# Optimization experiments

Hardware: AMD Instinct MI355X
Metric: run time of the kernel (lower is better)

The kernel has to match this reference:

```python
import jax, jax.numpy as jnp
import numpy as np

EPS = 1e-6  # torch.pairwise_distance default eps

def _linear(x, w, b):
    return x @ w.T + b

def _patch_attend(x, patches):
    # x: [B, C]; patches: [B, C, S]
    # torch.pairwise_distance(x.view(B,C,1), patches) -> [B, S] (norm over C)
    d = jnp.sqrt(jnp.sum((x[:, :, None] - patches + EPS) ** 2, axis=1))  # [B,S]
    p = jax.nn.softmax(jnp.exp(-d), axis=1)                              # [B,S]
    return jnp.einsum('bcs,bs->bc', patches, p)                          # [B,C]

def _get_D_and_A_m(HSI_D, LiDAR_D, data_HSI, data_LiDAR, m, K,
                   w1a, b1a, w2a, b2a):
    # Reconstructed get_D_and_A_m: cross-attention between batch features and
    # dictionary atoms using the attention net, with momentum dictionary update.
    # HSI_D, LiDAR_D: [30, D_num] (transposed dictionaries); data_*: [B, 30]
    # attention: H1 = lin1(H); D1 = lin2(D.T).T; H2 = lin1(H).T; D2 = lin2(D.T)
    H1_h = _linear(data_HSI, w1a, b1a)          # [B,60]
    D2_h = _linear(HSI_D.T, w2a, b2a)           # [D_num,60]
    S_h = H1_h @ D2_h.T                          # [B, D_num]
    A_h = jax.nn.softmax(S_h, axis=1)            # [B, D_num]
    out_h = A_h @ HSI_D.T                        # [B, 30]
    newD_h = m * HSI_D + (1.0 - m) * (data_HSI.T @ A_h)  # [30, D_num]

    H1_l = _linear(data_LiDAR, w1a, b1a)
    D2_l = _linear(LiDAR_D.T, w2a, b2a)
    S_l = H1_l @ D2_l.T
    A_l = jax.nn.softmax(S_l, axis=1)
    out_l = A_l @ LiDAR_D.T
    newD_l = m * LiDAR_D + (1.0 - m) * (data_LiDAR.T @ A_l)

    # A returned transposed ([60?]) -- model does HSI_A = HSI_A.T then cat dim=1
    # and out expects 120 features => A here must be [60, B]-like. We project
    # attended output through lin1 to get 60-dim features, transpose for return.
    feat_h = _linear(out_h, w1a, b1a).T          # [60, B]
    feat_l = _linear(out_l, w1a, b1a).T          # [60, B]
    return out_h, feat_h, newD_h, out_l, feat_l, newD_l

def setup_inputs():
    key = jax.random.key(0)
    ks = jax.random.split(key, 24)
    f = jax.random.normal
    inp = {
        'H_HSI': f(ks[0], (16384, 63), jnp.float32),
        'H_LiDAR': f(ks[1], (16384, 1), jnp.float32),
        'HSI_D': f(ks[2], (64, 63), jnp.float32),
        'LiDAR_D': f(ks[3], (64, 1), jnp.float32),
        'Patch_HSI': f(ks[4], (16384, 63, 49), jnp.float32),
        'Patch_LiDAR': f(ks[5], (16384, 1, 49), jnp.float32),
        'D_Patch_HSI': f(ks[6], (64, 63, 49), jnp.float32),
        'D_Patch_LiDAR': f(ks[7], (64, 1, 49), jnp.float32),
        'K': 10, 'm': 1, 'batchsize': 16384, 'D_num': 64,
    }
    def lin(k, o, i):
        k1, k2 = jax.random.split(k)
        s = 1.0 / np.sqrt(i)
        return (jax.random.uniform(k1, (o, i), jnp.float32, -s, s),
                jax.random.uniform(k2, (o,), jnp.float32, -s, s))
    inp['w1_1'], inp['b1_1'] = lin(ks[8], 45, 63)
    inp['w1_2'], inp['b1_2'] = lin(ks[9], 30, 45)
    inp['w2_1'], inp['b2_1'] = lin(ks[10], 15, 1)
    inp['w2_2'], inp['b2_2'] = lin(ks[11], 30, 15)
    inp['wa1'], inp['ba1'] = lin(ks[12], 60, 30)
    inp['wa2'], inp['ba2'] = lin(ks[13], 60, 30)
    inp['wo1'], inp['bo1'] = lin(ks[14], 60, 120)
    inp['wo2'], inp['bo2'] = lin(ks[15], 7, 60)
    return inp

def reference(H_HSI, H_LiDAR, HSI_D, LiDAR_D, Patch_HSI, Patch_LiDAR,
              D_Patch_HSI, D_Patch_LiDAR, K, m, batchsize, D_num,
              w1_1, b1_1, w1_2, b1_2, w2_1, b2_1, w2_2, b2_2,
              wa1, ba1, wa2, ba2, wo1, bo1, wo2, bo2):
    # patch attention aggregation for each branch
    SP_HSI = _patch_attend(H_HSI.reshape(H_HSI.shape[0], -1), Patch_HSI)
    SP_LiDAR = _patch_attend(H_LiDAR.reshape(H_LiDAR.shape[0], -1), Patch_LiDAR)
    D_SP_HSI = _patch_attend(HSI_D.reshape(HSI_D.shape[0], -1), D_Patch_HSI)
    D_SP_LiDAR = _patch_attend(LiDAR_D.reshape(LiDAR_D.shape[0], -1), D_Patch_LiDAR)

    lin1 = lambda x: _linear(_linear(x, w1_1, b1_1), w1_2, b1_2)  # 63->30
    lin2 = lambda x: _linear(_linear(x, w2_1, b2_1), w2_2, b2_2)  # 1->30

    data_HSI = lin1(SP_HSI)          # [B,30]
    data_LiDAR = lin2(SP_LiDAR)      # [B,30]
    HSI_Dp = lin1(D_SP_HSI).T        # [30,D_num]
    LiDAR_Dp = lin2(D_SP_LiDAR).T    # [30,D_num]

    mf = jnp.float32(m)
    out_h, HSI_A, HSI_Dn, out_l, LiDAR_A, LiDAR_Dn = _get_D_and_A_m(
        HSI_Dp, LiDAR_Dp, data_HSI, data_LiDAR, mf, K, wa1, ba1, wa2, ba2)

    HSI_A = HSI_A.T      # [B,60]
    LiDAR_A = LiDAR_A.T  # [B,60]
    A = jnp.concatenate([LiDAR_A, HSI_A], axis=1)  # [B,120]
    output = _linear(_linear(A, wo1, bo1), wo2, bo2)  # [B,Classes]
    return (data_HSI, data_LiDAR, HSI_A, HSI_Dn, LiDAR_A, LiDAR_Dn, output)
```

## Files before the change

kernel.cpp:

```cpp
#include <hip/hip_runtime.h>
#include <math.h>

#define NB 16384
#define DN 64
#define ST 68
#define OFF1 491520
#define OFF2 983040
#define OFF3 1966080
#define OFF4 1968000
#define OFF5 2951040
#define OFF6 2952960
#define SPH_OFF  0
#define SPL_OFF  1048576
#define DSPH_OFF 1064960
#define DSPL_OFF 1069056
#define DPTH_OFF 1069120
#define DPTL_OFF 1071040
#define D2H_OFF  1072960
#define D2L_OFF  1076800
#define AH_OFF   1080640
#define AL_OFF   2129216

typedef const __attribute__((address_space(1))) void* gas_ptr;
typedef __attribute__((address_space(3))) void* las_ptr;

__device__ __forceinline__ float wredmax(float v) {
#pragma unroll
    for (int m = 32; m; m >>= 1) v = fmaxf(v, __shfl_xor(v, m, 64));
    return v;
}
__device__ __forceinline__ float wredsum(float v) {
#pragma unroll
    for (int m = 32; m; m >>= 1) v += __shfl_xor(v, m, 64);
    return v;
}

template<int CH>
__device__ __forceinline__ void load_chunk(const float* __restrict__ xrow, float* __restrict__ x) {
    const int NQ = CH >> 2;
#pragma unroll
    for (int q = 0; q < NQ; ++q) {
        float4 v = *(const float4*)(xrow + 4 * q);
        x[4 * q] = v.x; x[4 * q + 1] = v.y; x[4 * q + 2] = v.z; x[4 * q + 3] = v.w;
    }
#pragma unroll
    for (int j = NQ * 4; j < CH; ++j) x[j] = xrow[j];
}

template<int INS, int RS, int PER>
__device__ __forceinline__ void dlayer4(const float* __restrict__ W,
                                        const float* __restrict__ bias,
                                        const float* __restrict__ xb,
                                        float* __restrict__ yb,
                                        const int OUTS, const int o0,
                                        const float scale)
{
    float acc[PER];
#pragma unroll
    for (int k = 0; k < PER; ++k) {
        int oc = o0 + k; oc = oc < OUTS ? oc : OUTS - 1;
        acc[k] = bias ? bias[oc] : 0.0f;
    }
#pragma unroll
    for (int c0 = 0; c0 < INS; c0 += 16) {
        const int CHv = (INS - c0) < 16 ? (INS - c0) : 16;
        float x[16];
        if (CHv == 16) load_chunk<16>(xb + c0, x);
        else if (CHv == 15) load_chunk<15>(xb + c0, x);
        else if (CHv == 14) load_chunk<14>(xb + c0, x);
        else if (CHv == 13) load_chunk<13>(xb + c0, x);
        else if (CHv == 12) load_chunk<12>(xb + c0, x);
        else {
#pragma unroll
            for (int j = 0; j < 16; ++j) if (j < CHv) x[j] = xb[c0 + j];
        }
#pragma unroll
        for (int k = 0; k < PER; ++k) {
            int oc = o0 + k; oc = oc < OUTS ? oc : OUTS - 1;
            const float* Wr = W + oc * RS + c0;
            float a = acc[k];
#pragma unroll
            for (int j = 0; j < 16; ++j) if (j < CHv) a = fmaf(Wr[j], x[j], a);
            acc[k] = a;
        }
    }
#pragma unroll
    for (int k = 0; k < PER; ++k) {
        int o = o0 + k;
        if (o < OUTS) yb[o] = acc[k] * scale;
    }
}

template<int INS, int CS, int PER>
__device__ __forceinline__ void dlayerT4(const float* __restrict__ W,
                                         const float* __restrict__ xb,
                                         float* __restrict__ yb,
                                         const int OUTS, const int o0,
                                         const float scale)
{
    float acc[PER];
#pragma unroll
    for (int k = 0; k < PER; ++k) acc[k] = 0.0f;
#pragma unroll
    for (int c0 = 0; c0 < INS; c0 += 16) {
        float x[16];
        load_chunk<16>(xb + c0, x);
#pragma unroll
        for (int j = 0; j < 16; ++j) {
            const float* Wr = W + (c0 + j) * CS + o0;
#pragma unroll
            for (int k = 0; k < PER; ++k) acc[k] = fmaf(Wr[k], x[j], acc[k]);
        }
    }
#pragma unroll
    for (int k = 0; k < PER; ++k) {
        int o = o0 + k;
        if (o < OUTS) yb[o] = acc[k] * scale;
    }
}

__device__ __forceinline__ void softmax_exp4(const float* __restrict__ Sb,
                                             float* __restrict__ Qb,
                                             float* __restrict__ P,
                                             const int w, const int l)
{
    const float4* S4 = (const float4*)Sb;
    float4 m4 = S4[0];
#pragma unroll
    for (int q = 1; q < 16; ++q) {
        float4 v = S4[q];
        m4.x = fmaxf(m4.x, v.x); m4.y = fmaxf(m4.y, v.y);
        m4.z = fmaxf(m4.z, v.z); m4.w = fmaxf(m4.w, v.w);
    }
    const float mx = fmaxf(fmaxf(m4.x, m4.y), fmaxf(m4.z, m4.w));
    float4 sv = S4[w];
    float4 e;
    e.x = __expf(sv.x - mx); e.y = __expf(sv.y - mx);
    e.z = __expf(sv.z - mx); e.w = __expf(sv.w - mx);
    ((float4*)Qb)[w] = e;
    P[w * 64 + l] = (e.x + e.y) + (e.z + e.w);
}

__device__ __forceinline__ float inv16(const float* __restrict__ P, const int l)
{
    float s0 = P[l], s1 = P[64 + l], s2 = P[128 + l], s3 = P[192 + l];
#pragma unroll
    for (int g = 4; g < 16; g += 4) {
        s0 += P[g * 64 + l];
        s1 += P[(g + 1) * 64 + l];
        s2 += P[(g + 2) * 64 + l];
        s3 += P[(g + 3) * 64 + l];
    }
    return 1.0f / ((s0 + s1) + (s2 + s3));
}

__global__ __launch_bounds__(256) void patch_attend_kernel(
    const float* __restrict__ patchH, const float* __restrict__ xH,
    const float* __restrict__ patchL, const float* __restrict__ xL,
    float* __restrict__ spH, float* __restrict__ spL,
    const float* __restrict__ dpH, const float* __restrict__ dxH,
    const float* __restrict__ dpL, const float* __restrict__ dxL,
    float* __restrict__ dspH, float* __restrict__ dspL)
{
    __shared__ __align__(16) float ph[4 * 3087];
    __shared__ __align__(16) float pl_[4 * 49];
    __shared__ __align__(16) float xh[4 * 63];
    __shared__ float xls[4];
    __shared__ float pw[4 * 49];

    const int tid = threadIdx.x;
    const bool isD = blockIdx.x >= (NB / 4);
    const int b0 = (isD ? (blockIdx.x - NB / 4) : blockIdx.x) * 4;
    const float* PH = isD ? dpH : patchH;
    const float* XH = isD ? dxH : xH;
    const float* PL = isD ? dpL : patchL;
    const float* XL = isD ? dxL : xL;
    float* SH = isD ? dspH : spH;
    float* SL = isD ? dspL : spL;
    {
        const float4* s4 = (const float4*)(PH + (size_t)b0 * 3087);
        float4* d4 = (float4*)ph;
        for (int i = tid; i < 3087; i += 256) {
            __builtin_amdgcn_global_load_lds((gas_ptr)(const void*)(s4 + i),
                                             (las_ptr)(void*)(d4 + i), 16, 0, 0);
        }
        if (tid < 49) ((float4*)pl_)[tid] = ((const float4*)(PL + (size_t)b0 * 49))[tid];
        if (tid >= 64 && tid < 127) ((float4*)xh)[tid - 64] = ((const float4*)(XH + (size_t)b0 * 63))[tid - 64];
        if (tid == 255) *((float4*)xls) = *((const float4*)(XL + b0));
    }
    asm volatile("s_waitcnt vmcnt(0)" ::: "memory");
    __syncthreads();

    const int w = tid >> 6, l = tid & 63;
    const float* phw = ph + w * 3087;
    const float* plw = pl_ + w * 49;
    const float* xhw = xh + w * 63;
    const float xlw = xls[w];

    float eh = -INFINITY, el = -INFINITY;
    if (l < 49) {
        float acc = 0.f;
#pragma unroll
        for (int c = 0; c < 63; ++c) {
            float t = xhw[c] - phw[c * 49 + l] + 1e-6f;
            acc = fmaf(t, t, acc);
        }
        eh = __expf(-sqrtf(acc));
        float tl = xlw - plw[l] + 1e-6f;
        el = __expf(-fabsf(tl));
    }
    float mh = wredmax(eh), ml = wredmax(el);
    float qh = (l < 49) ? __expf(eh - mh) : 0.f;
    float ql = (l < 49) ? __expf(el - ml) : 0.f;
    float sh = wredsum(qh);
    float sl = wredsum(ql);
    if (l < 49) pw[w * 49 + l] = qh / sh;
    float spl_v = wredsum((l < 49) ? plw[l] * (ql / sl) : 0.f);
    if (l == 0) SL[b0 + w] = spl_v;
    __syncthreads();
    if (l < 63) {
        float acc = 0.f;
        const float* pww = pw + w * 49;
#pragma unroll
        for (int s = 0; s < 49; ++s) acc = fmaf(phw[l * 49 + s], pww[s], acc);
        SH[(size_t)(b0 + w) * 64 + l] = acc;
    }
}

__global__ __launch_bounds__(1024) void dict_chain_kernel(
    const float* __restrict__ dsph, const float* __restrict__ dspl,
    const float* __restrict__ w1_1, const float* __restrict__ b1_1,
    const float* __restrict__ w1_2, const float* __restrict__ b1_2,
    const float* __restrict__ w2_1, const float* __restrict__ b2_1,
    const float* __restrict__ w2_2, const float* __restrict__ b2_2,
    const float* __restrict__ wa2, const float* __restrict__ ba2,
    float* __restrict__ dptH, float* __restrict__ dptL,
    float* __restrict__ d2H, float* __restrict__ d2L,
    const int* __restrict__ mI, float* __restrict__ out)
{
    __shared__ __align__(16) float HA[64 * ST];
    __shared__ __align__(16) float HB[64 * ST];
    __shared__ __align__(16) float LA[64 * ST];
    __shared__ __align__(16) float LB[64 * ST];
    __shared__ float XLs[64];
    const int tid = threadIdx.x;
    const int w = __builtin_amdgcn_readfirstlane(tid >> 6);
    const int l = tid & 63;
    const float mf = (float)(*mI);
    {
        int r = tid >> 4, q = tid & 15;
        *(float4*)(HA + r * ST + 4 * q) = ((const float4*)dsph)[tid];
        if (tid < 64) XLs[tid] = dspl[tid];
    }
    __syncthreads();
    dlayer4<63, 63, 3>(w1_1, b1_1, HA + l * ST, HB + l * ST, 45, w * 3, 1.0f);
    dlayer4<1, 1, 1>(w2_1, b2_1, XLs + l, LA + l * ST, 15, w, 1.0f);
    __syncthreads();
    dlayer4<45, 45, 2>(w1_2, b1_2, HB + l * ST, HA + l * ST, 30, w * 2, 1.0f);
    dlayer4<15, 15, 2>(w2_2, b2_2, LA + l * ST, LB + l * ST, 30, w * 2, 1.0f);
    __syncthreads();
    for (int i = tid; i < 1920; i += 1024) {
        int r = i / 30, c = i - r * 30;
        dptH[i] = HA[r * ST + c];
        dptL[i] = LB[r * ST + c];
    }
    for (int i = tid; i < 1920; i += 1024) {
        int c = i >> 6, j = i & 63;
        out[OFF3 + i] = mf * HA[j * ST + c];
        out[OFF5 + i] = mf * LB[j * ST + c];
    }
    dlayer4<30, 30, 4>(wa2, ba2, HA + l * ST, HB + l * ST, 60, w * 4, 1.0f);
    dlayer4<30, 30, 4>(wa2, ba2, LB + l * ST, LA + l * ST, 60, w * 4, 1.0f);
    __syncthreads();
    for (int i = tid; i < 3840; i += 1024) {
        int r = i / 60, c = i - r * 60;
        d2H[i] = HB[r * ST + c];
        d2L[i] = LA[r * ST + c];
    }
}

__global__ __launch_bounds__(1024) void chain_kernel(
    const float* __restrict__ spH, const float* __restrict__ spL,
    const float* __restrict__ dptH, const float* __restrict__ dptL,
    const float* __restrict__ d2H, const float* __restrict__ d2L,
    const float* __restrict__ w1_1, const float* __restrict__ b1_1,
    const float* __restrict__ w1_2, const float* __restrict__ b1_2,
    const float* __restrict__ w2_1, const float* __restrict__ b2_1,
    const float* __restrict__ w2_2, const float* __restrict__ b2_2,
    const float* __restrict__ wa1, const float* __restrict__ ba1,
    const float* __restrict__ wo1, const float* __restrict__ bo1,
    const float* __restrict__ wo2, const float* __restrict__ bo2,
    const int* __restrict__ mI,
    float* __restrict__ out, float* __restrict__ aH, float* __restrict__ aL)
{
    __shared__ __align__(16) float HA[64 * ST];
    __shared__ __align__(16) float HB[64 * ST];
    __shared__ __align__(16) float LA[64 * ST];
    __shared__ __align__(16) float LB[64 * ST];
    __shared__ float XLs[64];
    __shared__ float PH[16 * 64], PL[16 * 64];

    const int tid = threadIdx.x;
    const int w = __builtin_amdgcn_readfirstlane(tid >> 6);
    const int l = tid & 63;
    const int b0 = blockIdx.x * 64;
    const int b = b0 + l;
    const float mf = (float)(*mI);

    {
        int r = tid >> 4, q = tid & 15;
        *(float4*)(HA + r * ST + 4 * q) = ((const float4*)(spH + (size_t)b0 * 64))[tid];
        if (tid < 64) XLs[tid] = spL[b0 + tid];
    }
    __syncthreads();

    dlayer4<63, 63, 3>(w1_1, b1_1, HA + l * ST, HB + l * ST, 45, w * 3, 1.0f);
    dlayer4<1, 1, 1>(w2_1, b2_1, XLs + l, LA + l * ST, 15, w, 1.0f);
    __syncthreads();
    dlayer4<45, 45, 2>(w1_2, b1_2, HB + l * ST, HA + l * ST, 30, w * 2, 1.0f);
    dlayer4<15, 15, 2>(w2_2, b2_2, LA + l * ST, LB + l * ST, 30, w * 2, 1.0f);
    __syncthreads();
    for (int i = tid; i < 1920; i += 1024) {
        int r = i / 30, c = i - r * 30;
        out[(size_t)b0 * 30 + i] = HA[r * ST + c];
        out[OFF1 + (size_t)b0 * 30 + i] = LB[r * ST + c];
    }
    dlayer4<30, 30, 4>(wa1, ba1, HA + l * ST, HB + l * ST, 60, w * 4, 1.0f);
    dlayer4<30, 30, 4>(wa1, ba1, LB + l * ST, LA + l * ST, 60, w * 4, 1.0f);
    __syncthreads();
    dlayer4<60, 60, 4>(d2H, nullptr, HB + l * ST, HA + l * ST, 64, w * 4, 1.0f);
    dlayer4<60, 60, 4>(d2L, nullptr, LA + l * ST, LB + l * ST, 64, w * 4, 1.0f);
    __syncthreads();
    softmax_exp4(HA + l * ST, HB + l * ST, PH, w, l);
    softmax_exp4(LB + l * ST, LA + l * ST, PL, w, l);
    __syncthreads();
    if (mf != 1.0f) {
        for (int i = tid; i < 4096; i += 1024) {
            int r = i >> 6, j = i & 63;
            aH[(size_t)b0 * 64 + i] = HB[r * ST + j] * inv16(PH, r);
            aL[(size_t)b0 * 64 + i] = LA[r * ST + j] * inv16(PL, r);
        }
    }
    {
        const float invH = inv16(PH, l);
        const float invL = inv16(PL, l);
        dlayerT4<64, 30, 2>(dptH, HB + l * ST, HA + l * ST, 30, w * 2, invH);
        dlayerT4<64, 30, 2>(dptL, LA + l * ST, LB + l * ST, 30, w * 2, invL);
    }
    __syncthreads();
    dlayer4<30, 30, 4>(wa1, ba1, HA + l * ST, HB + l * ST, 60, w * 4, 1.0f);
    dlayer4<30, 30, 4>(wa1, ba1, LB + l * ST, LA + l * ST, 60, w * 4, 1.0f);
    __syncthreads();
    for (int i = tid; i < 3840; i += 1024) {
        int r = i / 60, c = i - r * 60;
        out[OFF2 + (size_t)b0 * 60 + i] = HB[r * ST + c];
        out[OFF4 + (size_t)b0 * 60 + i] = LA[r * ST + c];
    }
    {
        const int o0 = w * 4;
        float acc[4];
#pragma unroll
        for (int k = 0; k < 4; ++k) acc[k] = (o0 + k < 60) ? bo1[o0 + k] : 0.0f;
#pragma unroll
        for (int c0 = 0; c0 < 60; c0 += 16) {
            const int CH = (60 - c0) < 16 ? (60 - c0) : 16;
            float x[16];
            if (CH == 16) load_chunk<16>(LA + l * ST + c0, x);
            else load_chunk<12>(LA + l * ST + c0, x);
#pragma unroll
            for (int k = 0; k < 4; ++k) {
                int oc = o0 + k; oc = oc < 60 ? oc : 59;
                const float* Wr = wo1 + oc * 120 + c0;
                float a = acc[k];
#pragma unroll
                for (int j = 0; j < 16; ++j) if (j < CH) a = fmaf(Wr[j], x[j], a);
                acc[k] = a;
            }
        }
#pragma unroll
        for (int c0 = 0; c0 < 60; c0 += 16) {
            const int CH = (60 - c0) < 16 ? (60 - c0) : 16;
            float x[16];
            if (CH == 16) load_chunk<16>(HB + l * ST + c0, x);
            else load_chunk<12>(HB + l * ST + c0, x);
#pragma unroll
            for (int k = 0; k < 4; ++k) {
                int oc = o0 + k; oc = oc < 60 ? oc : 59;
                const float* Wr = wo1 + oc * 120 + 60 + c0;
                float a = acc[k];
#pragma unroll
                for (int j = 0; j < 16; ++j) if (j < CH) a = fmaf(Wr[j], x[j], a);
                acc[k] = a;
            }
        }
        if (o0 < 60) {
            float4 av; av.x = acc[0]; av.y = acc[1]; av.z = acc[2]; av.w = acc[3];
            *((float4*)(HA + l * ST + o0)) = av;
        }
    }
    __syncthreads();
    if (w < 7) {
        float a = bo2[w];
        const float* Wr = wo2 + w * 60;
#pragma unroll
        for (int c0 = 0; c0 < 60; c0 += 16) {
            const int CH = (60 - c0) < 16 ? (60 - c0) : 16;
            float x[16];
            if (CH == 16) load_chunk<16>(HA + l * ST + c0, x);
            else load_chunk<12>(HA + l * ST + c0, x);
#pragma unroll
            for (int j = 0; j < 16; ++j) if (j < CH) a = fmaf(Wr[c0 + j], x[j], a);
        }
        out[OFF6 + (size_t)b * 7 + w] = a;
    }
}

__global__ __launch_bounds__(256) void momentum_kernel(
    const float* __restrict__ dataH, const float* __restrict__ dataL,
    const float* __restrict__ aH, const float* __restrict__ aL,
    const int* __restrict__ mI, float* __restrict__ out)
{
    const float mf = (float)(*mI);
    if (mf == 1.0f) return;
    const int tid = threadIdx.x;
    const int chunk = blockIdx.x & 63;
    const int mod = blockIdx.x >> 6;
    const float* data = mod ? dataL : dataH;
    const float* A = mod ? aL : aH;
    float* D = out + (mod ? OFF5 : OFF3);
    const int b0 = chunk * 256;
    const int j = tid & 63;
    const int g = tid >> 6;
    float acc[8];
#pragma unroll
    for (int k = 0; k < 8; ++k) acc[k] = 0.f;
    for (int bb = 0; bb < 256; ++bb) {
        float a = A[(size_t)(b0 + bb) * 64 + j];
#pragma unroll
        for (int k = 0; k < 8; ++k) {
            int c = g + 4 * k; c = c < 30 ? c : 29;
            acc[k] = fmaf(data[(size_t)(b0 + bb) * 30 + c], a, acc[k]);
        }
    }
    const float s = 1.0f - mf;
#pragma unroll
    for (int k = 0; k < 8; ++k) {
        int c = g + 4 * k;
        if (c < 30) atomicAdd(&D[c * 64 + j], s * acc[k]);
    }
}

extern "C" void kernel_launch(void* const* d_in, const int* in_sizes, int n_in,
                              void* d_out, int out_size, void* d_ws, size_t ws_size,
                              hipStream_t stream) {
    const float* H_HSI        = (const float*)d_in[0];
    const float* H_LiDAR      = (const float*)d_in[1];
    const float* HSI_D        = (const float*)d_in[2];
    const float* LiDAR_D      = (const float*)d_in[3];
    const float* Patch_HSI    = (const float*)d_in[4];
    const float* Patch_LiDAR  = (const float*)d_in[5];
    const float* D_Patch_HSI  = (const float*)d_in[6];
    const float* D_Patch_LiDAR= (const float*)d_in[7];
    const int*   mI           = (const int*)d_in[9];
    const float* w1_1 = (const float*)d_in[12];
    const float* b1_1 = (const float*)d_in[13];
    const float* w1_2 = (const float*)d_in[14];
    const float* b1_2 = (const float*)d_in[15];
    const float* w2_1 = (const float*)d_in[16];
    const float* b2_1 = (const float*)d_in[17];
    const float* w2_2 = (const float*)d_in[18];
    const float* b2_2 = (const float*)d_in[19];
    const float* wa1  = (const float*)d_in[20];
    const float* ba1  = (const float*)d_in[21];
    const float* wa2  = (const float*)d_in[22];
    const float* ba2  = (const float*)d_in[23];
    const float* wo1  = (const float*)d_in[24];
    const float* bo1  = (const float*)d_in[25];
    const float* wo2  = (const float*)d_in[26];
    const float* bo2  = (const float*)d_in[27];

    float* out = (float*)d_out;
    float* ws  = (float*)d_ws;

    patch_attend_kernel<<<NB / 4 + DN / 4, 256, 0, stream>>>(
        Patch_HSI, H_HSI, Patch_LiDAR, H_LiDAR, ws + SPH_OFF, ws + SPL_OFF,
        D_Patch_HSI, HSI_D, D_Patch_LiDAR, LiDAR_D, ws + DSPH_OFF, ws + DSPL_OFF);
    dict_chain_kernel<<<1, 1024, 0, stream>>>(
        ws + DSPH_OFF, ws + DSPL_OFF,
        w1_1, b1_1, w1_2, b1_2, w2_1, b2_1, w2_2, b2_2, wa2, ba2,
        ws + DPTH_OFF, ws + DPTL_OFF, ws + D2H_OFF, ws + D2L_OFF, mI, out);
    chain_kernel<<<NB / 64, 1024, 0, stream>>>(
        ws + SPH_OFF, ws + SPL_OFF,
        ws + DPTH_OFF, ws + DPTL_OFF, ws + D2H_OFF, ws + D2L_OFF,
        w1_1, b1_1, w1_2, b1_2, w2_1, b2_1, w2_2, b2_2,
        wa1, ba1, wo1, bo1, wo2, bo2, mI,
        out, ws + AH_OFF, ws + AL_OFF);
    momentum_kernel<<<128, 256, 0, stream>>>(
        out, out + OFF1, ws + AH_OFF, ws + AL_OFF, mI, out);
}
```

Before: 84.49 us.

## Fold consecutive linear layers into precomputed combined weights in dict kernel

```diff
diff --git a/kernel.cpp b/kernel.cpp
--- a/kernel.cpp
+++ b/kernel.cpp
@@ -10,16 +10,24 @@
 #define OFF4 1968000
 #define OFF5 2951040
 #define OFF6 2952960
-#define SPH_OFF  0
-#define SPL_OFF  1048576
-#define DSPH_OFF 1064960
-#define DSPL_OFF 1069056
-#define DPTH_OFF 1069120
-#define DPTL_OFF 1071040
-#define D2H_OFF  1072960
-#define D2L_OFF  1076800
-#define AH_OFF   1080640
-#define AL_OFF   2129216
+#define SPH_OFF   0
+#define SPL_OFF   1048576
+#define DSPH_OFF  1064960
+#define DSPL_OFF  1069056
+#define W12H_OFF  1069120
+#define B12H_OFF  1071040
+#define W12L_OFF  1071072
+#define B12L_OFF  1071104
+#define MH_OFF    1071136
+#define B2H_OFF   1073056
+#define ML_OFF    1073120
+#define B2L_OFF   1075040
+#define GH_OFF    1075104
+#define GL_OFF    1078944
+#define WF_OFF    1082784
+#define BF_OFF    1083632
+#define AH_OFF    1083648
+#define AL_OFF    2132224
 
 typedef const __attribute__((address_space(1))) void* gas_ptr;
 typedef __attribute__((address_space(3))) void* las_ptr;
@@ -92,30 +100,39 @@
 }
 
 template<int INS, int CS, int PER>
-__device__ __forceinline__ void dlayerT4(const float* __restrict__ W,
-                                         const float* __restrict__ xb,
-                                         float* __restrict__ yb,
-                                         const int OUTS, const int o0,
-                                         const float scale)
+__device__ __forceinline__ void dlayerT4b(const float* __restrict__ W,
+                                          const float* __restrict__ bias,
+                                          const float* __restrict__ xb,
+                                          float* __restrict__ yb,
+                                          const int OUTS, const int o0,
+                                          const float scale)
 {
     float acc[PER];
 #pragma unroll
     for (int k = 0; k < PER; ++k) acc[k] = 0.0f;
 #pragma unroll
     for (int c0 = 0; c0 < INS; c0 += 16) {
+        const int CHv = (INS - c0) < 16 ? (INS - c0) : 16;
         float x[16];
-        load_chunk<16>(xb + c0, x);
+        if (CHv == 16) load_chunk<16>(xb + c0, x);
+        else if (CHv == 12) load_chunk<12>(xb + c0, x);
+        else {
+#pragma unroll
+            for (int j = 0; j < 16; ++j) if (j < CHv) x[j] = xb[c0 + j];
+        }
 #pragma unroll
         for (int j = 0; j < 16; ++j) {
-            const float* Wr = W + (c0 + j) * CS + o0;
-#pragma unroll
-            for (int k = 0; k < PER; ++k) acc[k] = fmaf(Wr[k], x[j], acc[k]);
+            if (j < CHv) {
+                const float* Wr = W + (c0 + j) * CS + o0;
+#pragma unroll
+                for (int k = 0; k < PER; ++k) acc[k] = fmaf(Wr[k], x[j], acc[k]);
+            }
         }
     }
 #pragma unroll
     for (int k = 0; k < PER; ++k) {
         int o = o0 + k;
-        if (o < OUTS) yb[o] = acc[k] * scale;
+        if (o < OUTS) yb[o] = bias ? (acc[k] * scale + bias[o]) : acc[k] * scale;
     }
 }
 
@@ -233,63 +250,108 @@
     const float* __restrict__ w1_2, const float* __restrict__ b1_2,
     const float* __restrict__ w2_1, const float* __restrict__ b2_1,
     const float* __restrict__ w2_2, const float* __restrict__ b2_2,
+    const float* __restrict__ wa1, const float* __restrict__ ba1,
     const float* __restrict__ wa2, const float* __restrict__ ba2,
-    float* __restrict__ dptH, float* __restrict__ dptL,
-    float* __restrict__ d2H, float* __restrict__ d2L,
+    const float* __restrict__ wo1, const float* __restrict__ bo1,
+    const float* __restrict__ wo2, const float* __restrict__ bo2,
+    float* __restrict__ w12H, float* __restrict__ b12H,
+    float* __restrict__ w12L, float* __restrict__ b12L,
+    float* __restrict__ mH, float* __restrict__ b2H,
+    float* __restrict__ mL, float* __restrict__ b2L,
+    float* __restrict__ gH, float* __restrict__ gL,
+    float* __restrict__ wf, float* __restrict__ bf,
     const int* __restrict__ mI, float* __restrict__ out)
 {
     __shared__ __align__(16) float HA[64 * ST];
     __shared__ __align__(16) float HB[64 * ST];
     __shared__ __align__(16) float LA[64 * ST];
     __shared__ __align__(16) float LB[64 * ST];
-    __shared__ float XLs[64];
+    __shared__ float W12s[1984];
+
     const int tid = threadIdx.x;
     const int w = __builtin_amdgcn_readfirstlane(tid >> 6);
     const int l = tid & 63;
     const float mf = (float)(*mI);
+    const float xl = dspl[l];
+
     {
         int r = tid >> 4, q = tid & 15;
         *(float4*)(HA + r * ST + 4 * q) = ((const float4*)dsph)[tid];
-        if (tid < 64) XLs[tid] = dspl[tid];
-    }
-    __syncthreads();
-    dlayer4<63, 63, 3>(w1_1, b1_1, HA + l * ST, HB + l * ST, 45, w * 3, 1.0f);
-    dlayer4<1, 1, 1>(w2_1, b2_1, XLs + l, LA + l * ST, 15, w, 1.0f);
-    __syncthreads();
-    dlayer4<45, 45, 2>(w1_2, b1_2, HB + l * ST, HA + l * ST, 30, w * 2, 1.0f);
-    dlayer4<15, 15, 2>(w2_2, b2_2, LA + l * ST, LB + l * ST, 30, w * 2, 1.0f);
-    __syncthreads();
-    for (int i = tid; i < 1920; i += 1024) {
-        int r = i / 30, c = i - r * 30;
-        dptH[i] = HA[r * ST + c];
-        dptL[i] = LB[r * ST + c];
-    }
+    }
+    for (int i = tid; i < 1890; i += 1024) {
+        int o = i / 63, c = i - o * 63;
+        float s = 0.f;
+        for (int k = 0; k < 45; ++k) s = fmaf(w1_2[o * 45 + k], w1_1[k * 63 + c], s);
+        W12s[i] = s; w12H[i] = s;
+    }
+    if (tid < 30) {
+        float s = b1_2[tid];
+        for (int k = 0; k < 45; ++k) s = fmaf(w1_2[tid * 45 + k], b1_1[k], s);
+        W12s[1890 + tid] = s; b12H[tid] = s;
+    }
+    if (tid >= 32 && tid < 62) {
+        int o = tid - 32;
+        float s = 0.f;
+        for (int k = 0; k < 15; ++k) s = fmaf(w2_2[o * 15 + k], w2_1[k], s);
+        W12s[1920 + o] = s; w12L[o] = s;
+    }
+    if (tid >= 64 && tid < 94) {
+        int o = tid - 64;
+        float s = b2_2[o];
+        for (int k = 0; k < 15; ++k) s = fmaf(w2_2[o * 15 + k], b2_1[k], s);
+        W12s[1950 + o] = s; b12L[o] = s;
+    }
+    for (int i = tid; i < 840; i += 1024) {
+        int o = i / 120, c = i - o * 120;
+        float s = 0.f;
+        for (int d = 0; d < 60; ++d) s = fmaf(wo2[o * 60 + d], wo1[d * 120 + c], s);
+        wf[i] = s;
+    }
+    if (tid >= 96 && tid < 103) {
+        int o = tid - 96;
+        float s = bo2[o];
+        for (int d = 0; d < 60; ++d) s = fmaf(wo2[o * 60 + d], bo1[d], s);
+        bf[o] = s;
+    }
+    __syncthreads();
+    dlayer4<63, 63, 2>(W12s, W12s + 1890, HA + l * ST, HB + l * ST, 30, w * 2, 1.0f);
+#pragma unroll
+    for (int k = 0; k < 2; ++k) {
+        int o = w * 2 + k;
+        if (o < 30) LB[l * ST + o] = fmaf(W12s[1920 + o], xl, W12s[1950 + o]);
+    }
+    __syncthreads();
     for (int i = tid; i < 1920; i += 1024) {
         int c = i >> 6, j = i & 63;
-        out[OFF3 + i] = mf * HA[j * ST + c];
+        out[OFF3 + i] = mf * HB[j * ST + c];
         out[OFF5 + i] = mf * LB[j * ST + c];
     }
-    dlayer4<30, 30, 4>(wa2, ba2, HA + l * ST, HB + l * ST, 60, w * 4, 1.0f);
+    dlayer4<30, 30, 4>(wa2, ba2, HB + l * ST, HA + l * ST, 60, w * 4, 1.0f);
     dlayer4<30, 30, 4>(wa2, ba2, LB + l * ST, LA + l * ST, 60, w * 4, 1.0f);
     __syncthreads();
-    for (int i = tid; i < 3840; i += 1024) {
-        int r = i / 60, c = i - r * 60;
-        d2H[i] = HB[r * ST + c];
-        d2L[i] = LA[r * ST + c];
+    dlayerT4b<60, 30, 2>(wa1, nullptr, HA + l * ST, mH + l * 30, 30, w * 2, 1.0f);
+    dlayerT4b<60, 30, 2>(wa1, nullptr, LA + l * ST, mL + l * 30, 30, w * 2, 1.0f);
+    dlayer4<30, 30, 4>(wa1, nullptr, HB + l * ST, gH + l * 60, 60, w * 4, 1.0f);
+    dlayer4<30, 30, 4>(wa1, nullptr, LB + l * ST, gL + l * 60, 60, w * 4, 1.0f);
+    if (tid < 64) {
+        float sH = 0.f, sL = 0.f;
+        for (int d = 0; d < 60; ++d) {
+            sH = fmaf(HA[tid * ST + d], ba1[d], sH);
+            sL = fmaf(LA[tid * ST + d], ba1[d], sL);
+        }
+        b2H[tid] = sH; b2L[tid] = sL;
     }
 }
 
 __global__ __launch_bounds__(1024) void chain_kernel(
     const float* __restrict__ spH, const float* __restrict__ spL,
-    const float* __restrict__ dptH, const float* __restrict__ dptL,
-    const float* __restrict__ d2H, const float* __restrict__ d2L,
-    const float* __restrict__ w1_1, const float* __restrict__ b1_1,
-    const float* __restrict__ w1_2, const float* __restrict__ b1_2,
-    const float* __restrict__ w2_1, const float* __restrict__ b2_1,
-    const float* __restrict__ w2_2, const float* __restrict__ b2_2,
-    const float* __restrict__ wa1, const float* __restrict__ ba1,
-    const float* __restrict__ wo1, const float* __restrict__ bo1,
-    const float* __restrict__ wo2, const float* __restrict__ bo2,
+    const float* __restrict__ w12H, const float* __restrict__ b12H,
+    const float* __restrict__ w12L, const float* __restrict__ b12L,
+    const float* __restrict__ mH, const float* __restrict__ b2H,
+    const float* __restrict__ mL, const float* __restrict__ b2L,
+    const float* __restrict__ gH, const float* __restrict__ gL,
+    const float* __restrict__ ba1,
+    const float* __restrict__ wf, const float* __restrict__ bf,
     const int* __restrict__ mI,
     float* __restrict__ out, float* __restrict__ aH, float* __restrict__ aL)
 {
@@ -297,7 +359,6 @@
     __shared__ __align__(16) float HB[64 * ST];
     __shared__ __align__(16) float LA[64 * ST];
     __shared__ __align__(16) float LB[64 * ST];
-    __shared__ float XLs[64];
     __shared__ float PH[16 * 64], PL[16 * 64];
 
     const int tid = threadIdx.x;
@@ -306,30 +367,28 @@
     const int b0 = blockIdx.x * 64;
     const int b = b0 + l;
     const float mf = (float)(*mI);
+    const float xl = spL[b];
 
     {
         int r = tid >> 4, q = tid & 15;
         *(float4*)(HA + r * ST + 4 * q) = ((const float4*)(spH + (size_t)b0 * 64))[tid];
-        if (tid < 64) XLs[tid] = spL[b0 + tid];
-    }
-    __syncthreads();
-
-    dlayer4<63, 63, 3>(w1_1, b1_1, HA + l * ST, HB + l * ST, 45, w * 3, 1.0f);
-    dlayer4<1, 1, 1>(w2_1, b2_1, XLs + l, LA + l * ST, 15, w, 1.0f);
-    __syncthreads();
-    dlayer4<45, 45, 2>(w1_2, b1_2, HB + l * ST, HA + l * ST, 30, w * 2, 1.0f);
-    dlayer4<15, 15, 2>(w2_2, b2_2, LA + l * ST, LB + l * ST, 30, w * 2, 1.0f);
+    }
+    __syncthreads();
+
+    dlayer4<63, 63, 2>(w12H, b12H, HA + l * ST, HB + l * ST, 30, w * 2, 1.0f);
+#pragma unroll
+    for (int k = 0; k < 2; ++k) {
+        int o = w * 2 + k;
+        if (o < 30) LA[l * ST + o] = fmaf(w12L[o], xl, b12L[o]);
+    }
     __syncthreads();
     for (int i = tid; i < 1920; i += 1024) {
         int r = i / 30, c = i - r * 30;
-        out[(size_t)b0 * 30 + i] = HA[r * ST + c];
-        out[OFF1 + (size_t)b0 * 30 + i] = LB[r * ST + c];
-    }
-    dlayer4<30, 30, 4>(wa1, ba1, HA + l * ST, HB + l * ST, 60, w * 4, 1.0f);
-    dlayer4<30, 30, 4>(wa1, ba1, LB + l * ST, LA + l * ST, 60, w * 4, 1.0f);
-    __syncthreads();
-    dlayer4<60, 60, 4>(d2H, nullptr, HB + l * ST, HA + l * ST, 64, w * 4, 1.0f);
-    dlayer4<60, 60, 4>(d2L, nullptr, LA + l * ST, LB + l * ST, 64, w * 4, 1.0f);
+        out[(size_t)b0 * 30 + i] = HB[r * ST + c];
+        out[OFF1 + (size_t)b0 * 30 + i] = LA[r * ST + c];
+    }
+    dlayer4<30, 30, 4>(mH, b2H, HB + l * ST, HA + l * ST, 64, w * 4, 1.0f);
+    dlayer4<30, 30, 4>(mL, b2L, LA + l * ST, LB + l * ST, 64, w * 4, 1.0f);
     __syncthreads();
     softmax_exp4(HA + l * ST, HB + l * ST, PH, w, l);
     softmax_exp4(LB + l * ST, LA + l * ST, PL, w, l);
@@ -344,64 +403,27 @@
     {
         const float invH = inv16(PH, l);
         const float invL = inv16(PL, l);
-        dlayerT4<64, 30, 2>(dptH, HB + l * ST, HA + l * ST, 30, w * 2, invH);
-        dlayerT4<64, 30, 2>(dptL, LA + l * ST, LB + l * ST, 30, w * 2, invL);
-    }
-    __syncthreads();
-    dlayer4<30, 30, 4>(wa1, ba1, HA + l * ST, HB + l * ST, 60, w * 4, 1.0f);
-    dlayer4<30, 30, 4>(wa1, ba1, LB + l * ST, LA + l * ST, 60, w * 4, 1.0f);
+        dlayerT4b<64, 60, 4>(gH, ba1, HB + l * ST, HA + l * ST, 60, w * 4, invH);
+        dlayerT4b<64, 60, 4>(gL, ba1, LA + l * ST, LB + l * ST, 60, w * 4, invL);
+    }
     __syncthreads();
     for (int i = tid; i < 3840; i += 1024) {
         int r = i / 60, c = i - r * 60;
-        out[OFF2 + (size_t)b0 * 60 + i] = HB[r * ST + c];
-        out[OFF4 + (size_t)b0 * 60 + i] = LA[r * ST + c];
-    }
-    {
-        const int o0 = w * 4;
-        float acc[4];
-#pragma unroll
-        for (int k = 0; k < 4; ++k) acc[k] = (o0 + k < 60) ? bo1[o0 + k] : 0.0f;
+        out[OFF2 + (size_t)b0 * 60 + i] = HA[r * ST + c];
+        out[OFF4 + (size_t)b0 * 60 + i] = LB[r * ST + c];
+    }
+    if (w < 7) {
+        float a = bf[w];
+        const float* Wr = wf + w * 120;
 #pragma unroll
         for (int c0 = 0; c0 < 60; c0 += 16) {
             const int CH = (60 - c0) < 16 ? (60 - c0) : 16;
             float x[16];
-            if (CH == 16) load_chunk<16>(LA + l * ST + c0, x);
-            else load_chunk<12>(LA + l * ST + c0, x);
-#pragma unroll
-            for (int k = 0; k < 4; ++k) {
-                int oc = o0 + k; oc = oc < 60 ? oc : 59;
-                const float* Wr = wo1 + oc * 120 + c0;
-                float a = acc[k];
-#pragma unroll
-                for (int j = 0; j < 16; ++j) if (j < CH) a = fmaf(Wr[j], x[j], a);
-                acc[k] = a;
-            }
-        }
-#pragma unroll
-        for (int c0 = 0; c0 < 60; c0 += 16) {
-            const int CH = (60 - c0) < 16 ? (60 - c0) : 16;
-            float x[16];
-            if (CH == 16) load_chunk<16>(HB + l * ST + c0, x);
-            else load_chunk<12>(HB + l * ST + c0, x);
-#pragma unroll
-            for (int k = 0; k < 4; ++k) {
-                int oc = o0 + k; oc = oc < 60 ? oc : 59;
-                const float* Wr = wo1 + oc * 120 + 60 + c0;
-                float a = acc[k];
-#pragma unroll
-                for (int j = 0; j < 16; ++j) if (j < CH) a = fmaf(Wr[j], x[j], a);
-                acc[k] = a;
-            }
-        }
-        if (o0 < 60) {
-            float4 av; av.x = acc[0]; av.y = acc[1]; av.z = acc[2]; av.w = acc[3];
-            *((float4*)(HA + l * ST + o0)) = av;
-        }
-    }
-    __syncthreads();
-    if (w < 7) {
-        float a = bo2[w];
-        const float* Wr = wo2 + w * 60;
+            if (CH == 16) load_chunk<16>(LB + l * ST + c0, x);
+            else load_chunk<12>(LB + l * ST + c0, x);
+#pragma unroll
+            for (int j = 0; j < 16; ++j) if (j < CH) a = fmaf(Wr[c0 + j], x[j], a);
+        }
 #pragma unroll
         for (int c0 = 0; c0 < 60; c0 += 16) {
             const int CH = (60 - c0) < 16 ? (60 - c0) : 16;
@@ -409,7 +431,7 @@
             if (CH == 16) load_chunk<16>(HA + l * ST + c0, x);
             else load_chunk<12>(HA + l * ST + c0, x);
 #pragma unroll
-            for (int j = 0; j < 16; ++j) if (j < CH) a = fmaf(Wr[c0 + j], x[j], a);
+            for (int j = 0; j < 16; ++j) if (j < CH) a = fmaf(Wr[60 + c0 + j], x[j], a);
         }
         out[OFF6 + (size_t)b * 7 + w] = a;
     }
@@ -487,14 +509,18 @@
         D_Patch_HSI, HSI_D, D_Patch_LiDAR, LiDAR_D, ws + DSPH_OFF, ws + DSPL_OFF);
     dict_chain_kernel<<<1, 1024, 0, stream>>>(
         ws + DSPH_OFF, ws + DSPL_OFF,
-        w1_1, b1_1, w1_2, b1_2, w2_1, b2_1, w2_2, b2_2, wa2, ba2,
-        ws + DPTH_OFF, ws + DPTL_OFF, ws + D2H_OFF, ws + D2L_OFF, mI, out);
+        w1_1, b1_1, w1_2, b1_2, w2_1, b2_1, w2_2, b2_2,
+        wa1, ba1, wa2, ba2, wo1, bo1, wo2, bo2,
+        ws + W12H_OFF, ws + B12H_OFF, ws + W12L_OFF, ws + B12L_OFF,
+        ws + MH_OFF, ws + B2H_OFF, ws + ML_OFF, ws + B2L_OFF,
+        ws + GH_OFF, ws + GL_OFF, ws + WF_OFF, ws + BF_OFF,
+        mI, out);
     chain_kernel<<<NB / 64, 1024, 0, stream>>>(
         ws + SPH_OFF, ws + SPL_OFF,
-        ws + DPTH_OFF, ws + DPTL_OFF, ws + D2H_OFF, ws + D2L_OFF,
-        w1_1, b1_1, w1_2, b1_2, w2_1, b2_1, w2_2, b2_2,
-        wa1, ba1, wo1, bo1, wo2, bo2, mI,
-        out, ws + AH_OFF, ws + AL_OFF);
+        ws + W12H_OFF, ws + B12H_OFF, ws + W12L_OFF, ws + B12L_OFF,
+        ws + MH_OFF, ws + B2H_OFF, ws + ML_OFF, ws + B2L_OFF,
+        ws + GH_OFF, ws + GL_OFF, ba1, ws + WF_OFF, ws + BF_OFF,
+        mI, out, ws + AH_OFF, ws + AL_OFF);
     momentum_kernel<<<128, 256, 0, stream>>>(
         out, out + OFF1, ws + AH_OFF, ws + AL_OFF, mI, out);
 }
```

New measurement: 108.6 us. 1.29x slower.

## Fuse momentum dictionary update into chain kernel via per-block atomics

Applied to the files above, without the earlier changes.

```diff
diff --git a/kernel.cpp b/kernel.cpp
--- a/kernel.cpp
+++ b/kernel.cpp
@@ -18,8 +18,6 @@
 #define DPTL_OFF 1071040
 #define D2H_OFF  1072960
 #define D2L_OFF  1076800
-#define AH_OFF   1080640
-#define AL_OFF   2129216
 
 typedef const __attribute__((address_space(1))) void* gas_ptr;
 typedef __attribute__((address_space(3))) void* las_ptr;
@@ -291,7 +289,7 @@
     const float* __restrict__ wo1, const float* __restrict__ bo1,
     const float* __restrict__ wo2, const float* __restrict__ bo2,
     const int* __restrict__ mI,
-    float* __restrict__ out, float* __restrict__ aH, float* __restrict__ aL)
+    float* __restrict__ out)
 {
     __shared__ __align__(16) float HA[64 * ST];
     __shared__ __align__(16) float HB[64 * ST];
@@ -299,6 +297,7 @@
     __shared__ __align__(16) float LB[64 * ST];
     __shared__ float XLs[64];
     __shared__ float PH[16 * 64], PL[16 * 64];
+    __shared__ float INVH[64], INVL[64];
 
     const int tid = threadIdx.x;
     const int w = __builtin_amdgcn_readfirstlane(tid >> 6);
@@ -335,10 +334,31 @@
     softmax_exp4(LB + l * ST, LA + l * ST, PL, w, l);
     __syncthreads();
     if (mf != 1.0f) {
-        for (int i = tid; i < 4096; i += 1024) {
-            int r = i >> 6, j = i & 63;
-            aH[(size_t)b0 * 64 + i] = HB[r * ST + j] * inv16(PH, r);
-            aL[(size_t)b0 * 64 + i] = LA[r * ST + j] * inv16(PL, r);
+        if (tid < 64) INVH[tid] = inv16(PH, tid);
+        else if (tid < 128) INVL[tid - 64] = inv16(PL, tid - 64);
+        __syncthreads();
+        const bool isH = w < 8;
+        const float* E = isH ? HB : LA;
+        const float* INV = isH ? INVH : INVL;
+        const float* dat = out + (isH ? 0 : OFF1) + (size_t)b0 * 30;
+        float* D = out + (isH ? OFF3 : OFF5);
+        const int c0 = (w & 7) * 4;
+        float acc[4];
+#pragma unroll
+        for (int k = 0; k < 4; ++k) acc[k] = 0.f;
+        for (int it = 0; it < 64; ++it) {
+            const float a = E[it * ST + l] * INV[it];
+#pragma unroll
+            for (int k = 0; k < 4; ++k) {
+                int c = c0 + k; c = c < 30 ? c : 29;
+                acc[k] = fmaf(dat[it * 30 + c], a, acc[k]);
+            }
+        }
+        const float s = 1.0f - mf;
+#pragma unroll
+        for (int k = 0; k < 4; ++k) {
+            int c = c0 + k;
+            if (c < 30) atomicAdd(&D[c * 64 + l], s * acc[k]);
         }
     }
     {
@@ -412,41 +432,6 @@
             for (int j = 0; j < 16; ++j) if (j < CH) a = fmaf(Wr[c0 + j], x[j], a);
         }
         out[OFF6 + (size_t)b * 7 + w] = a;
-    }
-}
-
-__global__ __launch_bounds__(256) void momentum_kernel(
-    const float* __restrict__ dataH, const float* __restrict__ dataL,
-    const float* __restrict__ aH, const float* __restrict__ aL,
-    const int* __restrict__ mI, float* __restrict__ out)
-{
-    const float mf = (float)(*mI);
-    if (mf == 1.0f) return;
-    const int tid = threadIdx.x;
-    const int chunk = blockIdx.x & 63;
-    const int mod = blockIdx.x >> 6;
-    const float* data = mod ? dataL : dataH;
-    const float* A = mod ? aL : aH;
-    float* D = out + (mod ? OFF5 : OFF3);
-    const int b0 = chunk * 256;
-    const int j = tid & 63;
-    const int g = tid >> 6;
-    float acc[8];
-#pragma unroll
-    for (int k = 0; k < 8; ++k) acc[k] = 0.f;
-    for (int bb = 0; bb < 256; ++bb) {
-        float a = A[(size_t)(b0 + bb) * 64 + j];
-#pragma unroll
-        for (int k = 0; k < 8; ++k) {
-            int c = g + 4 * k; c = c < 30 ? c : 29;
-            acc[k] = fmaf(data[(size_t)(b0 + bb) * 30 + c], a, acc[k]);
-        }
-    }
-    const float s = 1.0f - mf;
-#pragma unroll
-    for (int k = 0; k < 8; ++k) {
-        int c = g + 4 * k;
-        if (c < 30) atomicAdd(&D[c * 64 + j], s * acc[k]);
     }
 }
 
@@ -493,8 +478,5 @@
         ws + SPH_OFF, ws + SPL_OFF,
         ws + DPTH_OFF, ws + DPTL_OFF, ws + D2H_OFF, ws + D2L_OFF,
         w1_1, b1_1, w1_2, b1_2, w2_1, b2_1, w2_2, b2_2,
-        wa1, ba1, wo1, bo1, wo2, bo2, mI,
-        out, ws + AH_OFF, ws + AL_OFF);
-    momentum_kernel<<<128, 256, 0, stream>>>(
-        out, out + OFF1, ws + AH_OFF, ws + AL_OFF, mI, out);
-}
+        wa1, ba1, wo1, bo1, wo2, bo2, mI, out);
+}
```

After: 83.29 us. Within noise of the previous version (-1.4%).
